# Kernel optimization log

Measured on AMD Instinct MI355X. Metric: run time of the kernel, lower is better.

The kernel has to match this reference:

```python
import jax, jax.numpy as jnp
import numpy as np

N_NODES = 100_000
N_EDGES = 6_400_000
NUM_ELEMENTS = 4  # ['Cd','Se','S','Zn']
NUM_PAIRS = 10
CD_INDEX = 0
SE_INDEX = 1
# independent charge indices (all elements except Se, whose charge = -q_Cd)
INDEP_CHARGE_IDX = np.array([0, 2, 3], dtype=np.int64)


def setup_inputs() -> dict:
    key = jax.random.key(0)
    ks = jax.random.split(key, 10)
    raw_charges = jnp.array([1.18, -1.18, 1.18], dtype=jnp.float32)  # Cd, S, Zn
    A = jax.random.uniform(ks[0], (NUM_PAIRS,), minval=500.0, maxval=2000.0)
    rho = jax.random.uniform(ks[1], (NUM_PAIRS,), minval=0.2, maxval=0.5)
    C = jax.random.uniform(ks[2], (NUM_PAIRS,), minval=10.0, maxval=100.0)
    distances = jax.random.uniform(ks[3], (N_EDGES,), minval=1.5, maxval=6.0)
    inverse_distances_sq = 1.0 / (distances * distances)
    uv = jax.random.normal(ks[4], (N_EDGES, 3))
    edge_unit_vectors = uv / jnp.linalg.norm(uv, axis=1, keepdims=True)
    edge_index = jax.random.randint(ks[5], (2, N_EDGES), 0, N_NODES)
    pair_indices = jax.random.randint(ks[6], (N_EDGES,), 0, NUM_PAIRS)
    source_elements = jax.random.randint(ks[7], (N_EDGES,), 0, NUM_ELEMENTS)
    target_elements = jax.random.randint(ks[8], (N_EDGES,), 0, NUM_ELEMENTS)
    return {
        'raw_charges': raw_charges, 'A': A, 'rho': rho, 'C': C,
        'distances': distances, 'inverse_distances_sq': inverse_distances_sq,
        'edge_unit_vectors': edge_unit_vectors, 'edge_index': edge_index,
        'pair_indices': pair_indices, 'source_elements': source_elements,
        'target_elements': target_elements, 'n_nodes': N_NODES,
    }


def get_charges(raw_charges):
    # scatter independent charges, then enforce q_Se = -q_Cd
    charges = jnp.zeros((NUM_ELEMENTS,), dtype=raw_charges.dtype)
    charges = charges.at[INDEP_CHARGE_IDX].set(raw_charges)
    return charges.at[SE_INDEX].set(-charges[CD_INDEX])


def reference(raw_charges, A, rho, C, distances, inverse_distances_sq,
              edge_unit_vectors, edge_index, pair_indices,
              source_elements, target_elements, n_nodes):
    charges = get_charges(raw_charges)
    # gather per-edge pair parameters (Buckingham scalar force -dV/dr)
    A_p = A[pair_indices]
    rho_p = rho[pair_indices]
    C_p = C[pair_indices]
    inv_d2 = inverse_distances_sq
    potential_sf = (A_p / rho_p) * jnp.exp(-distances / rho_p) \
                   - 6.0 * C_p * inv_d2 * inv_d2 * inv_d2 / distances
    # Coulomb scalar force: q_i q_j / r^2
    coulomb_sf = charges[source_elements] * charges[target_elements] * inv_d2
    total_sf = potential_sf + coulomb_sf
    # per-edge force vectors, scatter-add to source atoms
    force_vectors = -total_sf[:, None] * edge_unit_vectors  # [E,3]
    forces = jax.ops.segment_sum(force_vectors, edge_index[0], num_segments=n_nodes)
    return forces
```

## Files before the change

### kernel.cpp

```cpp
#include <hip/hip_runtime.h>
#include <hip/hip_fp16.h>
#include <math.h>

#define NUM_PAIRS 10
#define BK_SHIFT 10
#define BK_NODES 1024
#define MAX_BK 128
#define EPB 4096
#define NCHUNK 4
#define CHUNK 1024

__device__ __forceinline__ void load_params(
    int t,
    const float* __restrict__ raw_charges,
    const float* __restrict__ A,
    const float* __restrict__ rho,
    const float* __restrict__ C,
    float* s_AoR, float* s_invRho, float* s_C6, float* s_qq)
{
    if (t < NUM_PAIRS) {
        float r = rho[t];
        float ir = 1.0f / r;
        s_invRho[t] = ir;
        s_AoR[t]    = A[t] * ir;
        s_C6[t]     = 6.0f * C[t];
    }
    if (t < 16) {
        float q0 = raw_charges[0];
        float qs0 = q0, qs1 = -q0, qs2 = raw_charges[1], qs3 = raw_charges[2];
        float qa = (t & 3) == 0 ? qs0 : (t & 3) == 1 ? qs1 : (t & 3) == 2 ? qs2 : qs3;
        int hb = t >> 2;
        float qb = hb == 0 ? qs0 : hb == 1 ? qs1 : hb == 2 ? qs2 : qs3;
        s_qq[t] = qa * qb;
    }
}

__device__ __forceinline__ float edge_force(
    float d, float inv_d2, int p, int se, int te,
    const float* s_AoR, const float* s_invRho, const float* s_C6, const float* s_qq)
{
    float inv_d  = inv_d2 * d;
    float inv_d6 = inv_d2 * inv_d2 * inv_d2;
    float pot  = s_AoR[p] * __expf(-d * s_invRho[p]) - s_C6[p] * inv_d6 * inv_d;
    float coul = s_qq[(te << 2) | se] * inv_d2;
    return pot + coul;
}

__device__ __forceinline__ uint2 pack_rec(float fx, float fy, float fz, int local) {
    unsigned hx = (unsigned)__half_as_ushort(__float2half(fx));
    unsigned hy = (unsigned)__half_as_ushort(__float2half(fy));
    unsigned hz = (unsigned)__half_as_ushort(__float2half(fz));
    uint2 r;
    r.x = hx | (hy << 16);
    r.y = hz | ((unsigned)local << 16);
    return r;
}

__global__ __launch_bounds__(256) void bin_kernel(
    const float* __restrict__ raw_charges,
    const float* __restrict__ A,
    const float* __restrict__ rho,
    const float* __restrict__ C,
    const float* __restrict__ distances,
    const float* __restrict__ uv,
    const int*   __restrict__ edge_src,
    const int*   __restrict__ pair_indices,
    const int*   __restrict__ src_elem,
    const int*   __restrict__ tgt_elem,
    int*   __restrict__ g_cnt,
    uint2* __restrict__ buf,
    int cap, int n_edges, int nb)
{
    __shared__ float s_AoR[NUM_PAIRS], s_invRho[NUM_PAIRS], s_C6[NUM_PAIRS], s_qq[16];
    __shared__ int hcnt[MAX_BK], hexcl[MAX_BK], gbase[MAX_BK];
    __shared__ int s_wsum[2];
    __shared__ uint2 s_rec[EPB];
    __shared__ unsigned char s_bb[EPB];

    const int t = threadIdx.x;
    load_params(t, raw_charges, A, rho, C, s_AoR, s_invRho, s_C6, s_qq);
    for (int k = t; k < nb; k += 256) hcnt[k] = 0;
    __syncthreads();

    const int blk_base = blockIdx.x * EPB;
    const bool full = (blk_base + EPB) <= n_edges;

    if (full) {
        uint2 rec[NCHUNK * 4];
        int   rkb[NCHUNK * 4];

#pragma unroll
        for (int c = 0; c < NCHUNK; ++c) {
            const int e0 = blk_base + c * CHUNK + t * 4;
            int4   src4 = *(const int4*)(edge_src + e0);
            float4 d4  = *(const float4*)(distances + e0);
            int4   p4  = *(const int4*)(pair_indices + e0);
            int4   se4 = *(const int4*)(src_elem + e0);
            int4   te4 = *(const int4*)(tgt_elem + e0);
            const float4* uvp = (const float4*)(uv + 3 * (size_t)e0);
            float4 u0 = uvp[0], u1 = uvp[1], u2 = uvp[2];

            float dd[4] = {d4.x, d4.y, d4.z, d4.w};
            int   pp[4] = {p4.x, p4.y, p4.z, p4.w};
            int   ss[4] = {se4.x, se4.y, se4.z, se4.w};
            int   tt[4] = {te4.x, te4.y, te4.z, te4.w};
            float ux[4] = {u0.x, u0.w, u1.z, u2.y};
            float uy[4] = {u0.y, u1.x, u1.w, u2.z};
            float uz[4] = {u0.z, u1.y, u2.x, u2.w};
            int   nd[4] = {src4.x, src4.y, src4.z, src4.w};

#pragma unroll
            for (int k = 0; k < 4; ++k) {
                float d = dd[k];
                float inv_d2 = 1.0f / (d * d);
                float tot = edge_force(d, inv_d2, pp[k], ss[k], tt[k],
                                       s_AoR, s_invRho, s_C6, s_qq);
                int j = c * 4 + k;
                int bb = nd[k] >> BK_SHIFT;
                rec[j] = pack_rec(-tot * ux[k], -tot * uy[k], -tot * uz[k],
                                  nd[k] & (BK_NODES - 1));
                rkb[j] = atomicAdd(&hcnt[bb], 1) | (bb << 16);
            }
        }
        __syncthreads();

        {
            const int w = t >> 6, lane = t & 63;
            int v = 0, sum = 0;
            if (t < 128) {
                v = (t < nb) ? hcnt[t] : 0;
                sum = v;
#pragma unroll
                for (int off = 1; off < 64; off <<= 1) {
                    int u = __shfl_up(sum, off, 64);
                    if (lane >= off) sum += u;
                }
                if (lane == 63) s_wsum[w] = sum;
            }
            __syncthreads();
            if (t < nb) {
                hexcl[t] = sum - v + (w ? s_wsum[0] : 0);
                gbase[t] = v ? atomicAdd(&g_cnt[t], v) : 0;
            }
            __syncthreads();
        }

#pragma unroll
        for (int j = 0; j < NCHUNK * 4; ++j) {
            int bb = rkb[j] >> 16;
            int idx = hexcl[bb] + (rkb[j] & 0xffff);
            s_rec[idx] = rec[j];
            s_bb[idx] = (unsigned char)bb;
        }
        __syncthreads();

#pragma unroll
        for (int k = 0; k < EPB / 256; ++k) {
            int i = t + k * 256;
            int bb = s_bb[i];
            int off = gbase[bb] + (i - hexcl[bb]);
            if (off < cap) buf[(size_t)bb * cap + off] = s_rec[i];
        }
    } else {
        for (int j = 0; j < EPB / 256; ++j) {
            int e = blk_base + j * 256 + t;
            if (e >= n_edges) continue;
            float d = distances[e];
            float inv_d2 = 1.0f / (d * d);
            float total = edge_force(d, inv_d2, pair_indices[e],
                                     src_elem[e], tgt_elem[e],
                                     s_AoR, s_invRho, s_C6, s_qq);
            float vx = uv[3 * (size_t)e + 0];
            float vy = uv[3 * (size_t)e + 1];
            float vz = uv[3 * (size_t)e + 2];
            int node = edge_src[e];
            int bb = node >> BK_SHIFT;
            int pos = atomicAdd(&g_cnt[bb], 1);
            if (pos < cap)
                buf[(size_t)bb * cap + pos] =
                    pack_rec(-total * vx, -total * vy, -total * vz,
                             node & (BK_NODES - 1));
        }
    }
}

template<int SLOTS>
__global__ __launch_bounds__(256) void gather_kernel(
    const uint2* __restrict__ buf,
    const int*   __restrict__ g_cnt,
    float* __restrict__ part,
    int cap)
{
    constexpr int KM = SLOTS / 256;
    __shared__ int   s_excl[BK_NODES];
    __shared__ int   s_wsum[4];
    __shared__ uint2 s_srt[SLOTS];

    const int s = blockIdx.x, S = gridDim.x, b = blockIdx.y;
    const int t = threadIdx.x;

    for (int k = t; k < BK_NODES; k += 256) s_excl[k] = 0;
    __syncthreads();

    int cnt = g_cnt[b];
    if (cnt > cap) cnt = cap;
    int lo = (int)((long)cnt * s / S);
    int hi = (int)((long)cnt * (s + 1) / S);

    const uint2* p = buf + (size_t)b * cap;

    uint2 rec[KM];
    int   rk[KM];
#pragma unroll
    for (int k = 0; k < KM; ++k) {
        int i = lo + t + k * 256;
        if (i < hi) rec[k] = p[i];
    }
#pragma unroll
    for (int k = 0; k < KM; ++k) {
        int i = lo + t + k * 256;
        if (i < hi) rk[k] = atomicAdd(&s_excl[rec[k].y >> 16], 1);
    }
    __syncthreads();

    int c0, c1, c2, c3;
    {
        int n0 = t << 2;
        c0 = s_excl[n0]; c1 = s_excl[n0 + 1]; c2 = s_excl[n0 + 2]; c3 = s_excl[n0 + 3];
        int tsum = c0 + c1 + c2 + c3;
        int lane = t & 63, w = t >> 6;
        int run = tsum;
#pragma unroll
        for (int off = 1; off < 64; off <<= 1) {
            int u = __shfl_up(run, off, 64);
            if (lane >= off) run += u;
        }
        if (lane == 63) s_wsum[w] = run;
        __syncthreads();
        int wbase = 0;
        if (w > 0) wbase += s_wsum[0];
        if (w > 1) wbase += s_wsum[1];
        if (w > 2) wbase += s_wsum[2];
        int base = wbase + run - tsum;
        s_excl[n0]     = base;
        s_excl[n0 + 1] = base + c0;
        s_excl[n0 + 2] = base + c0 + c1;
        s_excl[n0 + 3] = base + c0 + c1 + c2;
    }
    __syncthreads();

#pragma unroll
    for (int k = 0; k < KM; ++k) {
        int i = lo + t + k * 256;
        if (i < hi) {
            int node = rec[k].y >> 16;
            s_srt[s_excl[node] + rk[k]] = rec[k];
        }
    }
    __syncthreads();

    float out[12];
    int cq[4] = {c0, c1, c2, c3};
    int n0 = t << 2;
#pragma unroll
    for (int q = 0; q < 4; ++q) {
        int beg = s_excl[n0 + q], end = beg + cq[q];
        float fx = 0.f, fy = 0.f, fz = 0.f;
        for (int j = beg; j < end; ++j) {
            uint2 r = s_srt[j];
            fx += __half2float(__ushort_as_half((unsigned short)(r.x & 0xffff)));
            fy += __half2float(__ushort_as_half((unsigned short)(r.x >> 16)));
            fz += __half2float(__ushort_as_half((unsigned short)(r.y & 0xffff)));
        }
        out[q * 3 + 0] = fx; out[q * 3 + 1] = fy; out[q * 3 + 2] = fz;
    }
    float* op = part + ((size_t)b * S + s) * (BK_NODES * 3);
    float4* o4 = (float4*)op + t * 3;
    o4[0] = make_float4(out[0], out[1], out[2],  out[3]);
    o4[1] = make_float4(out[4], out[5], out[6],  out[7]);
    o4[2] = make_float4(out[8], out[9], out[10], out[11]);
}

__global__ __launch_bounds__(256) void reduce_kernel(
    const float4* __restrict__ part, float4* __restrict__ out, int n4, int S)
{
    int i = blockIdx.x * blockDim.x + threadIdx.x;
    if (i >= n4) return;
    int b = i / 768;
    int k = i - b * 768;
    const float4* p = part + (size_t)b * S * 768 + k;
    float4 s = make_float4(0.f, 0.f, 0.f, 0.f);
    for (int j = 0; j < S; ++j) {
        float4 v = p[(size_t)j * 768];
        s.x += v.x; s.y += v.y; s.z += v.z; s.w += v.w;
    }
    out[i] = s;
}

__global__ __launch_bounds__(256) void force_kernel_direct(
    const float* __restrict__ raw_charges,
    const float* __restrict__ A,
    const float* __restrict__ rho,
    const float* __restrict__ C,
    const float* __restrict__ distances,
    const float* __restrict__ uv,
    const int*   __restrict__ edge_src,
    const int*   __restrict__ pair_indices,
    const int*   __restrict__ src_elem,
    const int*   __restrict__ tgt_elem,
    float* __restrict__ forces,
    int n_edges)
{
    __shared__ float s_AoR[NUM_PAIRS], s_invRho[NUM_PAIRS], s_C6[NUM_PAIRS], s_qq[16];
    const int t = threadIdx.x;
    load_params(t, raw_charges, A, rho, C, s_AoR, s_invRho, s_C6, s_qq);
    __syncthreads();

    int e = blockIdx.x * blockDim.x + t;
    if (e >= n_edges) return;
    float d = distances[e];
    float inv_d2 = 1.0f / (d * d);
    float total = edge_force(d, inv_d2, pair_indices[e],
                             src_elem[e], tgt_elem[e], s_AoR, s_invRho, s_C6, s_qq);
    float ux = uv[3 * (size_t)e + 0], uy = uv[3 * (size_t)e + 1], uz = uv[3 * (size_t)e + 2];
    float* dst = forces + 3 * (size_t)edge_src[e];
    unsafeAtomicAdd(dst + 0, -total * ux);
    unsafeAtomicAdd(dst + 1, -total * uy);
    unsafeAtomicAdd(dst + 2, -total * uz);
}

extern "C" void kernel_launch(void* const* d_in, const int* in_sizes, int n_in,
                              void* d_out, int out_size, void* d_ws, size_t ws_size,
                              hipStream_t stream) {
    const float* raw_charges = (const float*)d_in[0];
    const float* A           = (const float*)d_in[1];
    const float* rho         = (const float*)d_in[2];
    const float* C           = (const float*)d_in[3];
    const float* distances   = (const float*)d_in[4];
    const float* uv          = (const float*)d_in[6];
    const int*   edge_index  = (const int*)d_in[7];
    const int*   pair_idx    = (const int*)d_in[8];
    const int*   src_elem    = (const int*)d_in[9];
    const int*   tgt_elem    = (const int*)d_in[10];

    float* forces = (float*)d_out;
    const int n_edges = in_sizes[4];
    const int n_out   = out_size;
    const int n_nodes = n_out / 3;

    const int B = 256;
    const int nb = (n_nodes + BK_NODES - 1) >> BK_SHIFT;

    long meanb = ((long)n_edges * BK_NODES) / (n_nodes > 0 ? n_nodes : 1);
    int cap = (int)(meanb + 8.0 * sqrt((double)(meanb > 0 ? meanb : 1)) + 256.0);
    cap = (cap + 255) & ~255;

    const size_t hdr = 8192;
    size_t off_buf = hdr;
    size_t sz_buf  = (size_t)nb * cap * sizeof(uint2);
    size_t off_part = (off_buf + sz_buf + 255) & ~(size_t)255;

    int S = 0, slots = 0;
    {
        size_t need16 = off_part + (size_t)nb * 16 * (BK_NODES * 3) * sizeof(float);
        size_t need32 = off_part + (size_t)nb * 32 * (BK_NODES * 3) * sizeof(float);
        if (ws_size >= need16 && (cap + 15) / 16 <= 4608)       { S = 16; slots = 4608; }
        else if (ws_size >= need32 && (cap + 31) / 32 <= 2304)  { S = 32; slots = 2304; }
    }

    if (nb <= MAX_BK && S > 0 && (n_out % 4) == 0) {
        int*   g_cnt = (int*)d_ws;
        uint2* buf   = (uint2*)((char*)d_ws + off_buf);
        float* part  = (float*)((char*)d_ws + off_part);

        hipMemsetAsync(g_cnt, 0, nb * sizeof(int), stream);

        int gridA = (n_edges + EPB - 1) / EPB;
        bin_kernel<<<gridA, B, 0, stream>>>(raw_charges, A, rho, C,
                                            distances, uv,
                                            edge_index, pair_idx, src_elem, tgt_elem,
                                            g_cnt, buf, cap, n_edges, nb);

        dim3 gridB(S, nb);
        if (slots == 4608)
            gather_kernel<4608><<<gridB, B, 0, stream>>>(buf, g_cnt, part, cap);
        else
            gather_kernel<2304><<<gridB, B, 0, stream>>>(buf, g_cnt, part, cap);

        int n4 = n_out / 4;
        reduce_kernel<<<(n4 + B - 1) / B, B, 0, stream>>>((const float4*)part,
                                                          (float4*)forces, n4, S);
    } else {
        hipMemsetAsync(forces, 0, (size_t)n_out * sizeof(float), stream);
        int grid = (n_edges + B - 1) / B;
        force_kernel_direct<<<grid, B, 0, stream>>>(raw_charges, A, rho, C,
                                                    distances, uv,
                                                    edge_index, pair_idx,
                                                    src_elem, tgt_elem,
                                                    forces, n_edges);
    }
}
```

Baseline: 300.3 us.

## Replace partial-sum buffer and reduce kernel with atomic adds into output

The gather kernel now atomically adds each node's per-slice partial force straight into the output array, so the per-slice partial buffer and the separate reduce kernel are gone. Zeroing of the output moves into the bin kernel as a grid-stride loop. This saves one kernel launch and the write and re-read of the partial buffer, at the cost of float atomics (16 slices contending per node) and the loss of deterministic summation order.

After: 453.4 us. +51.0%, slower.

```diff
diff --git a/kernel.cpp b/kernel.cpp
--- a/kernel.cpp
+++ b/kernel.cpp
@@ -69,6 +69,8 @@
     const int*   __restrict__ tgt_elem,
     int*   __restrict__ g_cnt,
     uint2* __restrict__ buf,
+    float* __restrict__ forces,
+    int n_out,
     int cap, int n_edges, int nb)
 {
     __shared__ float s_AoR[NUM_PAIRS], s_invRho[NUM_PAIRS], s_C6[NUM_PAIRS], s_qq[16];
@@ -78,6 +80,10 @@
     __shared__ unsigned char s_bb[EPB];
 
     const int t = threadIdx.x;
+
+    for (int i = blockIdx.x * 256 + t; i < n_out; i += gridDim.x * 256)
+        forces[i] = 0.0f;
+
     load_params(t, raw_charges, A, rho, C, s_AoR, s_invRho, s_C6, s_qq);
     for (int k = t; k < nb; k += 256) hcnt[k] = 0;
     __syncthreads();
@@ -188,7 +194,8 @@
 __global__ __launch_bounds__(256) void gather_kernel(
     const uint2* __restrict__ buf,
     const int*   __restrict__ g_cnt,
-    float* __restrict__ part,
+    float* __restrict__ forces,
+    int n_out,
     int cap)
 {
     constexpr int KM = SLOTS / 256;
@@ -259,7 +266,6 @@
     }
     __syncthreads();
 
-    float out[12];
     int cq[4] = {c0, c1, c2, c3};
     int n0 = t << 2;
 #pragma unroll
@@ -272,29 +278,13 @@
             fy += __half2float(__ushort_as_half((unsigned short)(r.x >> 16)));
             fz += __half2float(__ushort_as_half((unsigned short)(r.y & 0xffff)));
         }
-        out[q * 3 + 0] = fx; out[q * 3 + 1] = fy; out[q * 3 + 2] = fz;
-    }
-    float* op = part + ((size_t)b * S + s) * (BK_NODES * 3);
-    float4* o4 = (float4*)op + t * 3;
-    o4[0] = make_float4(out[0], out[1], out[2],  out[3]);
-    o4[1] = make_float4(out[4], out[5], out[6],  out[7]);
-    o4[2] = make_float4(out[8], out[9], out[10], out[11]);
-}
-
-__global__ __launch_bounds__(256) void reduce_kernel(
-    const float4* __restrict__ part, float4* __restrict__ out, int n4, int S)
-{
-    int i = blockIdx.x * blockDim.x + threadIdx.x;
-    if (i >= n4) return;
-    int b = i / 768;
-    int k = i - b * 768;
-    const float4* p = part + (size_t)b * S * 768 + k;
-    float4 s = make_float4(0.f, 0.f, 0.f, 0.f);
-    for (int j = 0; j < S; ++j) {
-        float4 v = p[(size_t)j * 768];
-        s.x += v.x; s.y += v.y; s.z += v.z; s.w += v.w;
-    }
-    out[i] = s;
+        int o = ((b << BK_SHIFT) + n0 + q) * 3;
+        if (o + 2 < n_out) {
+            unsafeAtomicAdd(&forces[o + 0], fx);
+            unsafeAtomicAdd(&forces[o + 1], fy);
+            unsafeAtomicAdd(&forces[o + 2], fz);
+        }
+    }
 }
 
 __global__ __launch_bounds__(256) void force_kernel_direct(
@@ -358,20 +348,15 @@
     const size_t hdr = 8192;
     size_t off_buf = hdr;
     size_t sz_buf  = (size_t)nb * cap * sizeof(uint2);
-    size_t off_part = (off_buf + sz_buf + 255) & ~(size_t)255;
+    size_t need    = off_buf + sz_buf;
 
     int S = 0, slots = 0;
-    {
-        size_t need16 = off_part + (size_t)nb * 16 * (BK_NODES * 3) * sizeof(float);
-        size_t need32 = off_part + (size_t)nb * 32 * (BK_NODES * 3) * sizeof(float);
-        if (ws_size >= need16 && (cap + 15) / 16 <= 4608)       { S = 16; slots = 4608; }
-        else if (ws_size >= need32 && (cap + 31) / 32 <= 2304)  { S = 32; slots = 2304; }
-    }
-
-    if (nb <= MAX_BK && S > 0 && (n_out % 4) == 0) {
+    if ((cap + 15) / 16 <= 4608)       { S = 16; slots = 4608; }
+    else if ((cap + 31) / 32 <= 2304)  { S = 32; slots = 2304; }
+
+    if (nb <= MAX_BK && S > 0 && ws_size >= need) {
         int*   g_cnt = (int*)d_ws;
         uint2* buf   = (uint2*)((char*)d_ws + off_buf);
-        float* part  = (float*)((char*)d_ws + off_part);
 
         hipMemsetAsync(g_cnt, 0, nb * sizeof(int), stream);
 
@@ -379,17 +364,14 @@
         bin_kernel<<<gridA, B, 0, stream>>>(raw_charges, A, rho, C,
                                             distances, uv,
                                             edge_index, pair_idx, src_elem, tgt_elem,
-                                            g_cnt, buf, cap, n_edges, nb);
+                                            g_cnt, buf, forces, n_out,
+                                            cap, n_edges, nb);
 
         dim3 gridB(S, nb);
         if (slots == 4608)
-            gather_kernel<4608><<<gridB, B, 0, stream>>>(buf, g_cnt, part, cap);
+            gather_kernel<4608><<<gridB, B, 0, stream>>>(buf, g_cnt, forces, n_out, cap);
         else
-            gather_kernel<2304><<<gridB, B, 0, stream>>>(buf, g_cnt, part, cap);
-
-        int n4 = n_out / 4;
-        reduce_kernel<<<(n4 + B - 1) / B, B, 0, stream>>>((const float4*)part,
-                                                          (float4*)forces, n4, S);
+            gather_kernel<2304><<<gridB, B, 0, stream>>>(buf, g_cnt, forces, n_out, cap);
     } else {
         hipMemsetAsync(forces, 0, (size_t)n_out * sizeof(float), stream);
         int grid = (n_edges + B - 1) / B;
```

## Drop shared-memory staging of binned records and double-buffer edge loads

Applied to the files above, without the earlier changes.

Records now go straight from registers to their global bucket slots, using each thread's local atomic rank plus the bucket's global base. This removes the block-level prefix scan, the shared staging arrays and two barriers. It also prefetches the next chunk's edge inputs while the current chunk is computed. The cost is scattered, uncoalesced global writes in place of sorted, contiguous ones, plus higher register pressure from the double-buffered input registers.

Result: slower. 314.7 us (+4.8%).

```diff
diff --git a/kernel.cpp b/kernel.cpp
--- a/kernel.cpp
+++ b/kernel.cpp
@@ -72,10 +72,7 @@
     int cap, int n_edges, int nb)
 {
     __shared__ float s_AoR[NUM_PAIRS], s_invRho[NUM_PAIRS], s_C6[NUM_PAIRS], s_qq[16];
-    __shared__ int hcnt[MAX_BK], hexcl[MAX_BK], gbase[MAX_BK];
-    __shared__ int s_wsum[2];
-    __shared__ uint2 s_rec[EPB];
-    __shared__ unsigned char s_bb[EPB];
+    __shared__ int hcnt[MAX_BK], gbase[MAX_BK];
 
     const int t = threadIdx.x;
     load_params(t, raw_charges, A, rho, C, s_AoR, s_invRho, s_C6, s_qq);
@@ -89,25 +86,44 @@
         uint2 rec[NCHUNK * 4];
         int   rkb[NCHUNK * 4];
 
+        int4   src4[2];
+        float4 d4[2];
+        int4   p4[2], se4[2], te4[2];
+        float4 u0[2], u1[2], u2[2];
+
+        {
+            const int e0 = blk_base + t * 4;
+            src4[0] = *(const int4*)(edge_src + e0);
+            d4[0]   = *(const float4*)(distances + e0);
+            p4[0]   = *(const int4*)(pair_indices + e0);
+            se4[0]  = *(const int4*)(src_elem + e0);
+            te4[0]  = *(const int4*)(tgt_elem + e0);
+            const float4* uvp = (const float4*)(uv + 3 * (size_t)e0);
+            u0[0] = uvp[0]; u1[0] = uvp[1]; u2[0] = uvp[2];
+        }
+
 #pragma unroll
         for (int c = 0; c < NCHUNK; ++c) {
-            const int e0 = blk_base + c * CHUNK + t * 4;
-            int4   src4 = *(const int4*)(edge_src + e0);
-            float4 d4  = *(const float4*)(distances + e0);
-            int4   p4  = *(const int4*)(pair_indices + e0);
-            int4   se4 = *(const int4*)(src_elem + e0);
-            int4   te4 = *(const int4*)(tgt_elem + e0);
-            const float4* uvp = (const float4*)(uv + 3 * (size_t)e0);
-            float4 u0 = uvp[0], u1 = uvp[1], u2 = uvp[2];
-
-            float dd[4] = {d4.x, d4.y, d4.z, d4.w};
-            int   pp[4] = {p4.x, p4.y, p4.z, p4.w};
-            int   ss[4] = {se4.x, se4.y, se4.z, se4.w};
-            int   tt[4] = {te4.x, te4.y, te4.z, te4.w};
-            float ux[4] = {u0.x, u0.w, u1.z, u2.y};
-            float uy[4] = {u0.y, u1.x, u1.w, u2.z};
-            float uz[4] = {u0.z, u1.y, u2.x, u2.w};
-            int   nd[4] = {src4.x, src4.y, src4.z, src4.w};
+            const int cur = c & 1, nxt = cur ^ 1;
+            if (c + 1 < NCHUNK) {
+                const int e1 = blk_base + (c + 1) * CHUNK + t * 4;
+                src4[nxt] = *(const int4*)(edge_src + e1);
+                d4[nxt]   = *(const float4*)(distances + e1);
+                p4[nxt]   = *(const int4*)(pair_indices + e1);
+                se4[nxt]  = *(const int4*)(src_elem + e1);
+                te4[nxt]  = *(const int4*)(tgt_elem + e1);
+                const float4* uvp = (const float4*)(uv + 3 * (size_t)e1);
+                u0[nxt] = uvp[0]; u1[nxt] = uvp[1]; u2[nxt] = uvp[2];
+            }
+
+            float dd[4] = {d4[cur].x, d4[cur].y, d4[cur].z, d4[cur].w};
+            int   pp[4] = {p4[cur].x, p4[cur].y, p4[cur].z, p4[cur].w};
+            int   ss[4] = {se4[cur].x, se4[cur].y, se4[cur].z, se4[cur].w};
+            int   tt[4] = {te4[cur].x, te4[cur].y, te4[cur].z, te4[cur].w};
+            float ux[4] = {u0[cur].x, u0[cur].w, u1[cur].z, u2[cur].y};
+            float uy[4] = {u0[cur].y, u1[cur].x, u1[cur].w, u2[cur].z};
+            float uz[4] = {u0[cur].z, u1[cur].y, u2[cur].x, u2[cur].w};
+            int   nd[4] = {src4[cur].x, src4[cur].y, src4[cur].z, src4[cur].w};
 
 #pragma unroll
             for (int k = 0; k < 4; ++k) {
@@ -124,42 +140,17 @@
         }
         __syncthreads();
 
-        {
-            const int w = t >> 6, lane = t & 63;
-            int v = 0, sum = 0;
-            if (t < 128) {
-                v = (t < nb) ? hcnt[t] : 0;
-                sum = v;
-#pragma unroll
-                for (int off = 1; off < 64; off <<= 1) {
-                    int u = __shfl_up(sum, off, 64);
-                    if (lane >= off) sum += u;
-                }
-                if (lane == 63) s_wsum[w] = sum;
-            }
-            __syncthreads();
-            if (t < nb) {
-                hexcl[t] = sum - v + (w ? s_wsum[0] : 0);
-                gbase[t] = v ? atomicAdd(&g_cnt[t], v) : 0;
-            }
-            __syncthreads();
-        }
+        if (t < nb) {
+            int v = hcnt[t];
+            gbase[t] = v ? atomicAdd(&g_cnt[t], v) : 0;
+        }
+        __syncthreads();
 
 #pragma unroll
         for (int j = 0; j < NCHUNK * 4; ++j) {
             int bb = rkb[j] >> 16;
-            int idx = hexcl[bb] + (rkb[j] & 0xffff);
-            s_rec[idx] = rec[j];
-            s_bb[idx] = (unsigned char)bb;
-        }
-        __syncthreads();
-
-#pragma unroll
-        for (int k = 0; k < EPB / 256; ++k) {
-            int i = t + k * 256;
-            int bb = s_bb[i];
-            int off = gbase[bb] + (i - hexcl[bb]);
-            if (off < cap) buf[(size_t)bb * cap + off] = s_rec[i];
+            int off = gbase[bb] + (rkb[j] & 0xffff);
+            if (off < cap) buf[(size_t)bb * cap + off] = rec[j];
         }
     } else {
         for (int j = 0; j < EPB / 256; ++j) {
```
